# Optimization experiments

Hardware: AMD Instinct MI355X
Metric: run time of the kernel (lower is better)

Reference implementation:

```python
import jax, jax.numpy as jnp
import numpy as np

NUM_HEADS = 6
EPS = 1e-6

def setup_inputs() -> dict:
    key = jax.random.key(0)
    k1, k2, k3, k4, k5 = jax.random.split(key, 5)
    B, N, C = 8, 1024, 384
    x = jax.random.normal(k1, (B, N, C), dtype=jnp.float32)
    # torch nn.Linear weights stored here as [in, out] for y = x @ W
    w_qkv = jax.random.normal(k2, (C, 3 * C), dtype=jnp.float32) * 0.02
    w_out = jax.random.normal(k3, (C, C), dtype=jnp.float32) * 0.02
    b_out = jax.random.normal(k4, (C,), dtype=jnp.float32) * 0.02
    # non-negative random-walk visitation mask (avg visits per node)
    mask = jax.random.uniform(k5, (N, N), dtype=jnp.float32)
    return {"x": x, "w_qkv": w_qkv, "w_out": w_out, "b_out": b_out, "mask": mask}

def reference(x, w_qkv, w_out, b_out, mask):
    B, N, C = x.shape
    H = NUM_HEADS
    D = C // H
    qkv = x @ w_qkv                                   # [B,N,3C]
    q, k, v = jnp.split(qkv, 3, axis=-1)
    # [B,N,C] -> [B,H,N,D]
    to_heads = lambda t: t.reshape(B, N, H, D).transpose(0, 2, 1, 3)
    q, k, v = to_heads(q), to_heads(k), to_heads(v)
    # feature map: relu(x) + eps
    q = jax.nn.relu(q) + EPS
    k = jax.nn.relu(k) + EPS
    # masked linear kernel: (Phi(Q) Phi(K)^T * mask)
    kernel = jnp.einsum("bhnd,bhmd->bhnm", q, k) * mask  # [B,H,N,N]
    z = 1.0 / (kernel.sum(axis=-1, keepdims=True) + EPS)  # row normalizer
    out = jnp.einsum("bhnm,bhmd->bhnd", kernel, v) * z    # [B,H,N,D]
    out = out.transpose(0, 2, 1, 3).reshape(B, N, C)
    return out @ w_out + b_out
```

## Files before the change

kernel.cpp:

```cpp
#include <hip/hip_runtime.h>
#include <hip/hip_bf16.h>
#include <hip/hip_fp16.h>
#include <stdint.h>

typedef __hip_bfloat16 bf16;
typedef __attribute__((ext_vector_type(8))) short short8;
typedef __attribute__((ext_vector_type(4))) float f32x4;
typedef __attribute__((ext_vector_type(16))) float f32x16;
typedef __attribute__((ext_vector_type(4))) int int4v;
typedef __attribute__((ext_vector_type(4))) unsigned short ushort4v;

#define MFMA16(A,B,C) __builtin_amdgcn_mfma_f32_16x16x32_bf16(A,B,C,0,0,0)
#define MFMA32(A,B,C) __builtin_amdgcn_mfma_f32_32x32x16_bf16(A,B,C,0,0,0)

static __device__ __forceinline__ void g2lds16(const void* g, void* l) {
  __builtin_amdgcn_global_load_lds(
      (__attribute__((address_space(1))) void*)(g),
      (__attribute__((address_space(3))) void*)(l), 16, 0, 0);
}

static __device__ __forceinline__ int swz8(int row, int kc) {
  return row * 8 + (kc ^ (row & 7));
}

static __device__ __forceinline__ unsigned short f2bf_bits(float f) {
  bf16 t = __float2bfloat16(f); unsigned short u; __builtin_memcpy(&u, &t, 2); return u;
}
static __device__ __forceinline__ unsigned short f2h_bits(float f) {
  __half t = __float2half(f); unsigned short u; __builtin_memcpy(&u, &t, 2); return u;
}

template<bool HALFOUT>
static __device__ __forceinline__ void tileT(const float* __restrict__ in,
                                             unsigned short* __restrict__ out,
                                             int R, int C, int tr, int tc, int tid,
                                             float (*tls)[65]) {
  const int rr0 = tid >> 4, c4 = tid & 15;
  #pragma unroll
  for (int rr = 0; rr < 4; ++rr) {
    int r = rr0 + rr * 16;
    float4 v = *(const float4*)(in + (size_t)(tr * 64 + r) * C + tc * 64 + c4 * 4);
    tls[r][c4 * 4 + 0] = v.x; tls[r][c4 * 4 + 1] = v.y;
    tls[r][c4 * 4 + 2] = v.z; tls[r][c4 * 4 + 3] = v.w;
  }
  __syncthreads();
  #pragma unroll
  for (int rr = 0; rr < 4; ++rr) {
    int r2 = rr0 + rr * 16;
    ushort4v o;
    #pragma unroll
    for (int k = 0; k < 4; ++k) {
      float f = tls[c4 * 4 + k][r2];
      o[k] = HALFOUT ? f2h_bits(f) : f2bf_bits(f);
    }
    *(ushort4v*)(out + (size_t)(tc * 64 + r2) * R + tr * 64 + c4 * 4) = o;
  }
}

__global__ __launch_bounds__(256)
void k_prep(const float* __restrict__ x, bf16* __restrict__ xb,
            const float* __restrict__ wqkv, unsigned short* __restrict__ wqkvT,
            const float* __restrict__ wout, unsigned short* __restrict__ woutT,
            const float* __restrict__ mask, unsigned short* __restrict__ maskT) {
  __shared__ float tls[64][65];
  const int bid = blockIdx.x, tid = threadIdx.x;
  if (bid < 768) {
    #pragma unroll
    for (int j = 0; j < 4; ++j) {
      int i = bid * 1024 + j * 256 + tid;
      float4 v = ((const float4*)x)[i];
      bf16* po = xb + (size_t)i * 4;
      po[0] = __float2bfloat16(v.x); po[1] = __float2bfloat16(v.y);
      po[2] = __float2bfloat16(v.z); po[3] = __float2bfloat16(v.w);
    }
  } else if (bid < 876) {
    int tt = bid - 768; tileT<false>(wqkv, wqkvT, 384, 1152, tt / 18, tt % 18, tid, tls);
  } else if (bid < 912) {
    int tt = bid - 876; tileT<false>(wout, woutT, 384, 384, tt / 6, tt % 6, tid, tls);
  } else {
    int tt = bid - 912; tileT<true>(mask, maskT, 1024, 1024, tt / 16, tt % 16, tid, tls);
  }
}

template<int EPI>
__global__ __launch_bounds__(256, 2)
void k_gemm(const bf16* __restrict__ A, const bf16* __restrict__ BT,
            bf16* __restrict__ Cb, float* __restrict__ Cf,
            const float* __restrict__ bias, bf16* __restrict__ vT,
            int M, int N, int K)
{
  __shared__ __align__(16) bf16 As[2][128 * 64];
  __shared__ __align__(16) bf16 Bs[2][128 * 64];
  const int tid = threadIdx.x;
  const int wave = tid >> 6, lane = tid & 63;
  const int lhi = lane >> 4, llo = lane & 15;
  const int wr = wave >> 1, wc = wave & 1;
  const int mBase = blockIdx.x * 128, nBase = blockIdx.y * 128;

  f32x4 acc[4][4] = {};

  auto stage = [&](int kt, int buf) {
    #pragma unroll
    for (int i = 0; i < 4; ++i) {
      int c = (wave * 4 + i) * 64 + lane;
      int row = c >> 3;
      int kc = (c & 7) ^ (row & 7);
      g2lds16(A  + (size_t)(mBase + row) * K + kt + kc * 8, As[buf] + (c & ~63) * 8);
      g2lds16(BT + (size_t)(nBase + row) * K + kt + kc * 8, Bs[buf] + (c & ~63) * 8);
    }
  };

  const int nT = K >> 6;
  stage(0, 0);
  __syncthreads();
  for (int t = 0; t < nT; ++t) {
    const int cur = t & 1;
    if (t + 1 < nT) stage((t + 1) << 6, cur ^ 1);
    for (int kk = 0; kk < 2; ++kk) {
      const int kc = kk * 4 + lhi;
      short8 a[4], b[4];
      #pragma unroll
      for (int mi = 0; mi < 4; ++mi)
        a[mi] = *(const short8*)(As[cur] + swz8(wr * 64 + mi * 16 + llo, kc) * 8);
      #pragma unroll
      for (int ni = 0; ni < 4; ++ni)
        b[ni] = *(const short8*)(Bs[cur] + swz8(wc * 64 + ni * 16 + llo, kc) * 8);
      #pragma unroll
      for (int mi = 0; mi < 4; ++mi)
        #pragma unroll
        for (int ni = 0; ni < 4; ++ni)
          acc[mi][ni] = MFMA16(a[mi], b[ni], acc[mi][ni]);
    }
    __syncthreads();
  }

  for (int mi = 0; mi < 4; ++mi)
    for (int ni = 0; ni < 4; ++ni) {
      const int colbase = nBase + wc * 64 + ni * 16;
      if (EPI == 1) {
        for (int j = 0; j < 4; ++j) {
          int row = mBase + wr * 64 + mi * 16 + lhi * 4 + j;
          int col = colbase + llo;
          Cf[(size_t)row * N + col] = acc[mi][ni][j] + bias[col];
        }
      } else if (colbase < 768) {
        for (int j = 0; j < 4; ++j) {
          int row = mBase + wr * 64 + mi * 16 + lhi * 4 + j;
          int col = colbase + llo;
          float v = fmaxf(acc[mi][ni][j], 0.f) + 1e-6f;
          Cb[(size_t)row * N + col] = __float2bfloat16(v);
        }
      } else {
        int col = colbase + llo;
        int dall = col - 768, hh = dall >> 6, dd = dall & 63;
        int rowg = mBase + wr * 64 + mi * 16 + lhi * 4;
        int bb = rowg >> 10, nloc = rowg & 1023;
        ushort4v pk;
        for (int j = 0; j < 4; ++j) pk[j] = f2bf_bits(acc[mi][ni][j]);
        *(ushort4v*)((unsigned short*)vT + (((size_t)bb * 6 + hh) * 64 + dd) * 1024 + nloc) = pk;
      }
    }
}

__global__ __launch_bounds__(256, 3)
void k_attn(const bf16* __restrict__ qkv,
            const bf16* __restrict__ vT,
            const __half* __restrict__ maskT,
            bf16* __restrict__ out)
{
  __shared__ __align__(16) bf16 Ks[2][64 * 64];
  __shared__ __align__(16) bf16 Vs[2][64 * 64];
  __shared__ float Ored[2][32][65];
  __shared__ float zred[2][2][32];

  const int bid = blockIdx.x;
  const int bh = bid % 48, qt = bid / 48;
  const int b = bh / 6, h = bh - b * 6;
  const int tid = threadIdx.x, wave = tid >> 6, lane = tid & 63;
  const int lq = lane & 31, lh = lane >> 5;
  const int wq = wave & 1, wm = wave >> 1;
  const size_t row0 = (size_t)b * 1024;
  const int qglob = qt * 64 + wq * 32 + lq;

  auto stageKV = [&](int mt, int buf) {
    #pragma unroll
    for (int i = 0; i < 2; ++i) {
      int c = (wave * 2 + i) * 64 + lane;
      int row = c >> 3;
      int kc = (c & 7) ^ (row & 7);
      g2lds16(qkv + (row0 + mt * 64 + row) * 1152 + 384 + h * 64 + kc * 8,
              Ks[buf] + (c & ~63) * 8);
      g2lds16(vT + ((size_t)bh * 64 + row) * 1024 + mt * 64 + kc * 8,
              Vs[buf] + (c & ~63) * 8);
    }
  };

  short8 bq[4];
  {
    const bf16* qp = qkv + (row0 + qglob) * 1152 + h * 64 + lh * 8;
    #pragma unroll
    for (int ks = 0; ks < 4; ++ks) bq[ks] = *(const short8*)(qp + ks * 16);
  }
  stageKV(0, 0);

  f32x16 accO[2] = {};
  float zl = 0.f;

  __syncthreads();

  #pragma unroll 1
  for (int mt = 0; mt < 16; ++mt) {
    const int cur = mt & 1;
    const bf16* Kc = Ks[cur];
    const bf16* Vc = Vs[cur];

    __half mv[16];
    {
      const int mrow0 = mt * 64 + wm * 32 + 4 * lh;
      #pragma unroll
      for (int g = 0; g < 4; ++g)
        #pragma unroll
        for (int j = 0; j < 4; ++j)
          mv[g * 4 + j] = maskT[(size_t)(mrow0 + 8 * g + j) * 1024 + qglob];
    }
    if (mt < 15) stageKV(mt + 1, cur ^ 1);

    f32x16 st = {};
    #pragma unroll
    for (int ks = 0; ks < 4; ++ks) {
      int row = wm * 32 + lq;
      int cc = (ks * 2 + lh) ^ (row & 7);
      short8 af = *(const short8*)(Kc + (row * 8 + cc) * 8);
      st = MFMA32(af, bq[ks], st);
    }

    float p[16];
    {
      float zp = 0.f;
      #pragma unroll
      for (int r = 0; r < 16; ++r) {
        p[r] = st[r] * __half2float(mv[r]);
        zp += p[r];
      }
      zl += zp;
    }
    int u[4][2];
    #pragma unroll
    for (int g = 0; g < 4; ++g)
      #pragma unroll
      for (int c = 0; c < 2; ++c)
        asm("v_cvt_pk_bf16_f32 %0, %1, %2"
            : "=v"(u[g][c]) : "v"(p[4 * g + 2 * c]), "v"(p[4 * g + 2 * c + 1]));

    short8 pa[2];
    #pragma unroll
    for (int ks = 0; ks < 2; ++ks) {
      int A0 = u[2 * ks][0], A0b = u[2 * ks][1];
      int A1 = u[2 * ks + 1][0], A1b = u[2 * ks + 1][1];
      int x0 = __shfl_xor(A0, 32), x1 = __shfl_xor(A0b, 32);
      int y0 = __shfl_xor(A1, 32), y1 = __shfl_xor(A1b, 32);
      int4v iv;
      iv.x = lh ? y0 : A0;
      iv.y = lh ? y1 : A0b;
      iv.z = lh ? A1 : x0;
      iv.w = lh ? A1b : x1;
      pa[ks] = *(short8*)&iv;
    }

    #pragma unroll
    for (int db = 0; db < 2; ++db)
      #pragma unroll
      for (int ks = 0; ks < 2; ++ks) {
        int row = db * 32 + lq;
        int cc = (wm * 4 + ks * 2 + lh) ^ (row & 7);
        short8 vb = *(const short8*)(Vc + (row * 8 + cc) * 8);
        accO[db] = MFMA32(pa[ks], vb, accO[db]);
      }

    __syncthreads();
  }

  zl += __shfl_xor(zl, 32);
  zred[wq][wm][lq] = zl;
  if (wm == 1) {
    #pragma unroll
    for (int db = 0; db < 2; ++db)
      #pragma unroll
      for (int r = 0; r < 16; ++r) {
        int q = (r & 3) + 8 * (r >> 2) + 4 * lh;
        Ored[wq][q][db * 32 + lq] = accO[db][r];
      }
  }
  __syncthreads();
  if (wm == 0) {
    #pragma unroll
    for (int r = 0; r < 16; ++r) {
      int q = (r & 3) + 8 * (r >> 2) + 4 * lh;
      float zt = zred[wq][0][q] + zred[wq][1][q];
      float zi = 1.f / (zt + 1e-6f);
      int n = qt * 64 + wq * 32 + q;
      size_t orow = (row0 + n) * 384 + h * 64;
      #pragma unroll
      for (int db = 0; db < 2; ++db) {
        float val = (accO[db][r] + Ored[wq][q][db * 32 + lq]) * zi;
        out[orow + db * 32 + lq] = __float2bfloat16(val);
      }
    }
  }
}

__global__ __launch_bounds__(256, 3)
void k_gemm_out(const bf16* __restrict__ A, const bf16* __restrict__ BT,
                float* __restrict__ Cf, const float* __restrict__ bias)
{
  __shared__ __align__(16) bf16 As[2][64 * 64];
  __shared__ __align__(16) bf16 Bs[2][64 * 64];
  const int tid = threadIdx.x;
  const int wave = tid >> 6, lane = tid & 63;
  const int lq = lane & 31, lh = lane >> 5;
  const int wr = wave >> 1, wc = wave & 1;
  const int mBase = blockIdx.x * 64, nBase = blockIdx.y * 64;
  const int N = 384, K = 384;

  auto stage = [&](int kt, int buf) {
    #pragma unroll
    for (int i = 0; i < 2; ++i) {
      int c = (wave * 2 + i) * 64 + lane;
      int row = c >> 3;
      int kc = (c & 7) ^ (row & 7);
      g2lds16(A  + (size_t)(mBase + row) * K + kt + kc * 8, As[buf] + (c & ~63) * 8);
      g2lds16(BT + (size_t)(nBase + row) * K + kt + kc * 8, Bs[buf] + (c & ~63) * 8);
    }
  };

  f32x16 acc = {};
  const int nT = K >> 6;
  stage(0, 0);
  __syncthreads();
  for (int t = 0; t < nT; ++t) {
    const int cur = t & 1;
    if (t + 1 < nT) stage((t + 1) << 6, cur ^ 1);
    #pragma unroll
    for (int ks = 0; ks < 4; ++ks) {
      int ra = wr * 32 + lq, rb = wc * 32 + lq;
      short8 a = *(const short8*)(As[cur] + (ra * 8 + ((ks * 2 + lh) ^ (ra & 7))) * 8);
      short8 b = *(const short8*)(Bs[cur] + (rb * 8 + ((ks * 2 + lh) ^ (rb & 7))) * 8);
      acc = MFMA32(a, b, acc);
    }
    __syncthreads();
  }
  #pragma unroll
  for (int r = 0; r < 16; ++r) {
    int row = mBase + wr * 32 + (r & 3) + 8 * (r >> 2) + 4 * lh;
    int col = nBase + wc * 32 + lq;
    Cf[(size_t)row * N + col] = acc[r] + bias[col];
  }
}

extern "C" void kernel_launch(void* const* d_in, const int* in_sizes, int n_in,
                              void* d_out, int out_size, void* d_ws, size_t ws_size,
                              hipStream_t stream) {
  (void)in_sizes; (void)n_in; (void)out_size; (void)ws_size;
  const float* x    = (const float*)d_in[0];
  const float* wqkv = (const float*)d_in[1];
  const float* wout = (const float*)d_in[2];
  const float* bout = (const float*)d_in[3];
  const float* mask = (const float*)d_in[4];
  float* outp = (float*)d_out;

  char* ws = (char*)d_ws;
  bf16*  xb    = (bf16*)(ws);
  bf16*  wqkvT = (bf16*)(ws + 6291456);
  bf16*  woutT = (bf16*)(ws + 7176192);
  bf16*  qkvb  = (bf16*)(ws + 7471104);
  bf16*  vTb   = (bf16*)(ws + 26345472);
  bf16*  ab    = (bf16*)(ws + 32636928);
  __half* maskT = (__half*)(ws + 38928384);

  k_prep<<<dim3(1168), dim3(256), 0, stream>>>(
      x, xb, wqkv, (unsigned short*)wqkvT, wout, (unsigned short*)woutT,
      mask, (unsigned short*)maskT);

  k_gemm<0><<<dim3(64, 9), dim3(256), 0, stream>>>(xb, wqkvT, qkvb, nullptr, nullptr,
                                                   vTb, 8192, 1152, 384);
  k_attn<<<dim3(768), dim3(256), 0, stream>>>(qkvb, vTb, maskT, ab);
  k_gemm_out<<<dim3(128, 6), dim3(256), 0, stream>>>(ab, woutT, outp, bout);
}
```

Before: 64.96 us.

## Halve attention block to two waves each covering both query sub-tiles

The attention kernel now uses 128 threads (2 waves) instead of 4. Each wave processes both 32-query halves of the tile, so every K and V fragment read from LDS feeds two MFMAs. LDS for K/V staging is aliased with the reduction buffers to shrink the footprint. The aim is more data reuse and fewer redundant LDS reads, at the cost of roughly double the accumulator registers per wave, fewer waves per block to hide latency, and a launch bound of 2.

```diff
diff --git a/kernel.cpp b/kernel.cpp
--- a/kernel.cpp
+++ b/kernel.cpp
@@ -162,150 +162,161 @@
     }
 }
 
-__global__ __launch_bounds__(256, 3)
+__global__ __launch_bounds__(128, 2)
 void k_attn(const bf16* __restrict__ qkv,
             const bf16* __restrict__ vT,
             const __half* __restrict__ maskT,
             bf16* __restrict__ out)
 {
-  __shared__ __align__(16) bf16 Ks[2][64 * 64];
-  __shared__ __align__(16) bf16 Vs[2][64 * 64];
-  __shared__ float Ored[2][32][65];
-  __shared__ float zred[2][2][32];
+  __shared__ __align__(16) char smem[33280];
+  bf16* KsB = (bf16*)smem;
+  bf16* VsB = KsB + 8192;
+  float* OredF = (float*)smem;
+  float* zredF = (float*)(smem + 32768);
 
   const int bid = blockIdx.x;
   const int bh = bid % 48, qt = bid / 48;
   const int b = bh / 6, h = bh - b * 6;
-  const int tid = threadIdx.x, wave = tid >> 6, lane = tid & 63;
+  const int tid = threadIdx.x, wm = tid >> 6, lane = tid & 63;
   const int lq = lane & 31, lh = lane >> 5;
-  const int wq = wave & 1, wm = wave >> 1;
   const size_t row0 = (size_t)b * 1024;
-  const int qglob = qt * 64 + wq * 32 + lq;
 
   auto stageKV = [&](int mt, int buf) {
     #pragma unroll
-    for (int i = 0; i < 2; ++i) {
-      int c = (wave * 2 + i) * 64 + lane;
+    for (int i = 0; i < 4; ++i) {
+      int c = (wm * 4 + i) * 64 + lane;
       int row = c >> 3;
       int kc = (c & 7) ^ (row & 7);
       g2lds16(qkv + (row0 + mt * 64 + row) * 1152 + 384 + h * 64 + kc * 8,
-              Ks[buf] + (c & ~63) * 8);
+              KsB + buf * 4096 + (c & ~63) * 8);
       g2lds16(vT + ((size_t)bh * 64 + row) * 1024 + mt * 64 + kc * 8,
-              Vs[buf] + (c & ~63) * 8);
+              VsB + buf * 4096 + (c & ~63) * 8);
     }
   };
 
-  short8 bq[4];
-  {
-    const bf16* qp = qkv + (row0 + qglob) * 1152 + h * 64 + lh * 8;
-    #pragma unroll
-    for (int ks = 0; ks < 4; ++ks) bq[ks] = *(const short8*)(qp + ks * 16);
+  short8 bqf[2][4];
+  #pragma unroll
+  for (int bq2 = 0; bq2 < 2; ++bq2) {
+    const bf16* qp = qkv + (row0 + qt * 64 + bq2 * 32 + lq) * 1152 + h * 64 + lh * 8;
+    #pragma unroll
+    for (int ks = 0; ks < 4; ++ks) bqf[bq2][ks] = *(const short8*)(qp + ks * 16);
   }
   stageKV(0, 0);
 
-  f32x16 accO[2] = {};
-  float zl = 0.f;
+  f32x16 accO[2][2] = {};
+  float zl[2] = {};
 
   __syncthreads();
 
   #pragma unroll 1
   for (int mt = 0; mt < 16; ++mt) {
     const int cur = mt & 1;
-    const bf16* Kc = Ks[cur];
-    const bf16* Vc = Vs[cur];
-
-    __half mv[16];
-    {
-      const int mrow0 = mt * 64 + wm * 32 + 4 * lh;
+    const bf16* Kc = KsB + cur * 4096;
+    const bf16* Vc = VsB + cur * 4096;
+
+    __half mv[2][16];
+    const int mrow0 = mt * 64 + wm * 32 + 4 * lh;
+    #pragma unroll
+    for (int bq2 = 0; bq2 < 2; ++bq2) {
+      const int qg = qt * 64 + bq2 * 32 + lq;
       #pragma unroll
       for (int g = 0; g < 4; ++g)
         #pragma unroll
         for (int j = 0; j < 4; ++j)
-          mv[g * 4 + j] = maskT[(size_t)(mrow0 + 8 * g + j) * 1024 + qglob];
+          mv[bq2][g * 4 + j] = maskT[(size_t)(mrow0 + 8 * g + j) * 1024 + qg];
     }
     if (mt < 15) stageKV(mt + 1, cur ^ 1);
 
-    f32x16 st = {};
+    f32x16 st0 = {}, st1 = {};
     #pragma unroll
     for (int ks = 0; ks < 4; ++ks) {
       int row = wm * 32 + lq;
       int cc = (ks * 2 + lh) ^ (row & 7);
       short8 af = *(const short8*)(Kc + (row * 8 + cc) * 8);
-      st = MFMA32(af, bq[ks], st);
-    }
-
-    float p[16];
-    {
+      st0 = MFMA32(af, bqf[0][ks], st0);
+      st1 = MFMA32(af, bqf[1][ks], st1);
+    }
+
+    short8 pa[2][2];
+    #pragma unroll
+    for (int bq2 = 0; bq2 < 2; ++bq2) {
+      const f32x16& stc = bq2 ? st1 : st0;
+      float p[16];
       float zp = 0.f;
       #pragma unroll
       for (int r = 0; r < 16; ++r) {
-        p[r] = st[r] * __half2float(mv[r]);
+        p[r] = stc[r] * __half2float(mv[bq2][r]);
         zp += p[r];
       }
-      zl += zp;
-    }
-    int u[4][2];
-    #pragma unroll
-    for (int g = 0; g < 4; ++g)
-      #pragma unroll
-      for (int c = 0; c < 2; ++c)
-        asm("v_cvt_pk_bf16_f32 %0, %1, %2"
-            : "=v"(u[g][c]) : "v"(p[4 * g + 2 * c]), "v"(p[4 * g + 2 * c + 1]));
-
-    short8 pa[2];
-    #pragma unroll
-    for (int ks = 0; ks < 2; ++ks) {
-      int A0 = u[2 * ks][0], A0b = u[2 * ks][1];
-      int A1 = u[2 * ks + 1][0], A1b = u[2 * ks + 1][1];
-      int x0 = __shfl_xor(A0, 32), x1 = __shfl_xor(A0b, 32);
-      int y0 = __shfl_xor(A1, 32), y1 = __shfl_xor(A1b, 32);
-      int4v iv;
-      iv.x = lh ? y0 : A0;
-      iv.y = lh ? y1 : A0b;
-      iv.z = lh ? A1 : x0;
-      iv.w = lh ? A1b : x1;
-      pa[ks] = *(short8*)&iv;
+      zl[bq2] += zp;
+      int u[4][2];
+      #pragma unroll
+      for (int g = 0; g < 4; ++g)
+        #pragma unroll
+        for (int c = 0; c < 2; ++c)
+          asm("v_cvt_pk_bf16_f32 %0, %1, %2"
+              : "=v"(u[g][c]) : "v"(p[4 * g + 2 * c]), "v"(p[4 * g + 2 * c + 1]));
+      #pragma unroll
+      for (int ks2 = 0; ks2 < 2; ++ks2) {
+        int A0 = u[2 * ks2][0], A0b = u[2 * ks2][1];
+        int A1 = u[2 * ks2 + 1][0], A1b = u[2 * ks2 + 1][1];
+        int x0 = __shfl_xor(A0, 32), x1 = __shfl_xor(A0b, 32);
+        int y0 = __shfl_xor(A1, 32), y1 = __shfl_xor(A1b, 32);
+        int4v iv;
+        iv.x = lh ? y0 : A0;
+        iv.y = lh ? y1 : A0b;
+        iv.z = lh ? A1 : x0;
+        iv.w = lh ? A1b : x1;
+        pa[bq2][ks2] = *(short8*)&iv;
+      }
     }
 
     #pragma unroll
     for (int db = 0; db < 2; ++db)
       #pragma unroll
-      for (int ks = 0; ks < 2; ++ks) {
+      for (int ks2 = 0; ks2 < 2; ++ks2) {
         int row = db * 32 + lq;
-        int cc = (wm * 4 + ks * 2 + lh) ^ (row & 7);
+        int cc = (wm * 4 + ks2 * 2 + lh) ^ (row & 7);
         short8 vb = *(const short8*)(Vc + (row * 8 + cc) * 8);
-        accO[db] = MFMA32(pa[ks], vb, accO[db]);
+        accO[0][db] = MFMA32(pa[0][ks2], vb, accO[0][db]);
+        accO[1][db] = MFMA32(pa[1][ks2], vb, accO[1][db]);
       }
 
     __syncthreads();
   }
 
-  zl += __shfl_xor(zl, 32);
-  zred[wq][wm][lq] = zl;
+  zl[0] += __shfl_xor(zl[0], 32);
+  zl[1] += __shfl_xor(zl[1], 32);
+  zredF[wm * 64 + lq] = zl[0];
+  zredF[wm * 64 + 32 + lq] = zl[1];
   if (wm == 1) {
     #pragma unroll
-    for (int db = 0; db < 2; ++db)
+    for (int bq2 = 0; bq2 < 2; ++bq2)
+      #pragma unroll
+      for (int db = 0; db < 2; ++db)
+        #pragma unroll
+        for (int r = 0; r < 16; ++r) {
+          int ql = bq2 * 32 + (r & 3) + 8 * (r >> 2) + 4 * lh;
+          OredF[ql * 66 + db * 32 + lq] = accO[bq2][db][r];
+        }
+  }
+  __syncthreads();
+  if (wm == 0) {
+    #pragma unroll
+    for (int bq2 = 0; bq2 < 2; ++bq2)
       #pragma unroll
       for (int r = 0; r < 16; ++r) {
-        int q = (r & 3) + 8 * (r >> 2) + 4 * lh;
-        Ored[wq][q][db * 32 + lq] = accO[db][r];
-      }
-  }
-  __syncthreads();
-  if (wm == 0) {
-    #pragma unroll
-    for (int r = 0; r < 16; ++r) {
-      int q = (r & 3) + 8 * (r >> 2) + 4 * lh;
-      float zt = zred[wq][0][q] + zred[wq][1][q];
-      float zi = 1.f / (zt + 1e-6f);
-      int n = qt * 64 + wq * 32 + q;
-      size_t orow = (row0 + n) * 384 + h * 64;
-      #pragma unroll
-      for (int db = 0; db < 2; ++db) {
-        float val = (accO[db][r] + Ored[wq][q][db * 32 + lq]) * zi;
-        out[orow + db * 32 + lq] = __float2bfloat16(val);
-      }
-    }
+        int ql = bq2 * 32 + (r & 3) + 8 * (r >> 2) + 4 * lh;
+        float zt = zredF[ql] + zredF[64 + ql];
+        float zi = 1.f / (zt + 1e-6f);
+        int n = qt * 64 + ql;
+        size_t orow = (row0 + n) * 384 + h * 64;
+        #pragma unroll
+        for (int db = 0; db < 2; ++db) {
+          float val = (accO[bq2][db][r] + OredF[ql * 66 + db * 32 + lq]) * zi;
+          out[orow + db * 32 + lq] = __float2bfloat16(val);
+        }
+      }
   }
 }
 
@@ -383,6 +394,6 @@
 
   k_gemm<0><<<dim3(64, 9), dim3(256), 0, stream>>>(xb, wqkvT, qkvb, nullptr, nullptr,
                                                    vTb, 8192, 1152, 384);
-  k_attn<<<dim3(768), dim3(256), 0, stream>>>(qkvb, vTb, maskT, ab);
+  k_attn<<<dim3(768), dim3(128), 0, stream>>>(qkvb, vTb, maskT, ab);
   k_gemm_out<<<dim3(128, 6), dim3(256), 0, stream>>>(ab, woutT, outp, bout);
 }
```

Result: slower. 70.12 us (+7.9%).

## Single-buffer K/V in LDS via register staging and alias reduction scratch

Applied to the files above, without the earlier changes.

The attention kernel drops double-buffered direct global-to-LDS loads. Each K/V tile is now prefetched into registers at the top of the iteration and written to a single LDS buffer after compute, with the epilogue's reduction arrays aliased onto the same shared memory. Shared memory per block falls from about 49KB to 17KB, which is meant to let more blocks stay resident per CU. The cost is an extra barrier per iteration, more registers held for the prefetch, and LDS writes issued from VGPRs.

```diff
diff --git a/kernel.cpp b/kernel.cpp
--- a/kernel.cpp
+++ b/kernel.cpp
@@ -168,10 +168,11 @@
             const __half* __restrict__ maskT,
             bf16* __restrict__ out)
 {
-  __shared__ __align__(16) bf16 Ks[2][64 * 64];
-  __shared__ __align__(16) bf16 Vs[2][64 * 64];
-  __shared__ float Ored[2][32][65];
-  __shared__ float zred[2][2][32];
+  __shared__ __align__(16) char smem[17408];
+  bf16* Ks = (bf16*)smem;
+  bf16* Vs = Ks + 4096;
+  float* OredF = (float*)smem;
+  float* zredF = (float*)(smem + 16896);
 
   const int bid = blockIdx.x;
   const int bh = bid % 48, qt = bid / 48;
@@ -182,16 +183,23 @@
   const size_t row0 = (size_t)b * 1024;
   const int qglob = qt * 64 + wq * 32 + lq;
 
-  auto stageKV = [&](int mt, int buf) {
+  int4v kreg[2], vreg[2];
+  auto stage_load = [&](int mt) {
     #pragma unroll
     for (int i = 0; i < 2; ++i) {
       int c = (wave * 2 + i) * 64 + lane;
-      int row = c >> 3;
-      int kc = (c & 7) ^ (row & 7);
-      g2lds16(qkv + (row0 + mt * 64 + row) * 1152 + 384 + h * 64 + kc * 8,
-              Ks[buf] + (c & ~63) * 8);
-      g2lds16(vT + ((size_t)bh * 64 + row) * 1024 + mt * 64 + kc * 8,
-              Vs[buf] + (c & ~63) * 8);
+      int row = c >> 3, kc = c & 7;
+      kreg[i] = *(const int4v*)(qkv + (row0 + mt * 64 + row) * 1152 + 384 + h * 64 + kc * 8);
+      vreg[i] = *(const int4v*)(vT + ((size_t)bh * 64 + row) * 1024 + mt * 64 + kc * 8);
+    }
+  };
+  auto stage_write = [&]() {
+    #pragma unroll
+    for (int i = 0; i < 2; ++i) {
+      int c = (wave * 2 + i) * 64 + lane;
+      int row = c >> 3, kc = c & 7;
+      *(int4v*)(Ks + swz8(row, kc) * 8) = kreg[i];
+      *(int4v*)(Vs + swz8(row, kc) * 8) = vreg[i];
     }
   };
 
@@ -201,18 +209,17 @@
     #pragma unroll
     for (int ks = 0; ks < 4; ++ks) bq[ks] = *(const short8*)(qp + ks * 16);
   }
-  stageKV(0, 0);
+
+  stage_load(0);
+  stage_write();
+  __syncthreads();
 
   f32x16 accO[2] = {};
   float zl = 0.f;
 
-  __syncthreads();
-
   #pragma unroll 1
   for (int mt = 0; mt < 16; ++mt) {
-    const int cur = mt & 1;
-    const bf16* Kc = Ks[cur];
-    const bf16* Vc = Vs[cur];
+    if (mt < 15) stage_load(mt + 1);
 
     __half mv[16];
     {
@@ -223,14 +230,13 @@
         for (int j = 0; j < 4; ++j)
           mv[g * 4 + j] = maskT[(size_t)(mrow0 + 8 * g + j) * 1024 + qglob];
     }
-    if (mt < 15) stageKV(mt + 1, cur ^ 1);
 
     f32x16 st = {};
     #pragma unroll
     for (int ks = 0; ks < 4; ++ks) {
       int row = wm * 32 + lq;
       int cc = (ks * 2 + lh) ^ (row & 7);
-      short8 af = *(const short8*)(Kc + (row * 8 + cc) * 8);
+      short8 af = *(const short8*)(Ks + (row * 8 + cc) * 8);
       st = MFMA32(af, bq[ks], st);
     }
 
@@ -273,22 +279,26 @@
       for (int ks = 0; ks < 2; ++ks) {
         int row = db * 32 + lq;
         int cc = (wm * 4 + ks * 2 + lh) ^ (row & 7);
-        short8 vb = *(const short8*)(Vc + (row * 8 + cc) * 8);
+        short8 vb = *(const short8*)(Vs + (row * 8 + cc) * 8);
         accO[db] = MFMA32(pa[ks], vb, accO[db]);
       }
 
     __syncthreads();
+    if (mt < 15) {
+      stage_write();
+      __syncthreads();
+    }
   }
 
   zl += __shfl_xor(zl, 32);
-  zred[wq][wm][lq] = zl;
+  zredF[(wq * 2 + wm) * 32 + lq] = zl;
   if (wm == 1) {
     #pragma unroll
     for (int db = 0; db < 2; ++db)
       #pragma unroll
       for (int r = 0; r < 16; ++r) {
         int q = (r & 3) + 8 * (r >> 2) + 4 * lh;
-        Ored[wq][q][db * 32 + lq] = accO[db][r];
+        OredF[(wq * 32 + q) * 65 + db * 32 + lq] = accO[db][r];
       }
   }
   __syncthreads();
@@ -296,13 +306,13 @@
     #pragma unroll
     for (int r = 0; r < 16; ++r) {
       int q = (r & 3) + 8 * (r >> 2) + 4 * lh;
-      float zt = zred[wq][0][q] + zred[wq][1][q];
+      float zt = zredF[wq * 2 * 32 + q] + zredF[(wq * 2 + 1) * 32 + q];
       float zi = 1.f / (zt + 1e-6f);
       int n = qt * 64 + wq * 32 + q;
       size_t orow = (row0 + n) * 384 + h * 64;
       #pragma unroll
       for (int db = 0; db < 2; ++db) {
-        float val = (accO[db][r] + Ored[wq][q][db * 32 + lq]) * zi;
+        float val = (accO[db][r] + OredF[(wq * 32 + q) * 65 + db * 32 + lq]) * zi;
         out[orow + db * 32 + lq] = __float2bfloat16(val);
       }
     }
```

Result: slower. 67.06 us (+3.2%).
